# Performance work log

Measured on AMD Instinct MI355X. Metric: run time of the kernel, lower is better.

Reference implementation:

```python
import jax, jax.numpy as jnp
import numpy as np

B, T, EMB = 2, 2048, 1024
H, D = 16, 64          # n_heads, head_dim; H*D == EMB
FF = 4 * EMB


def _ln(x, w, b, eps=1e-5):
    mu = jnp.mean(x, axis=-1, keepdims=True)
    var = jnp.var(x, axis=-1, keepdims=True)
    return (x - mu) * jax.lax.rsqrt(var + eps) * w + b


def setup_inputs() -> dict:
    key = jax.random.key(0)
    ks = jax.random.split(key, 5)
    s = 0.02
    return {
        "x": jax.random.normal(ks[0], (B, T, EMB), jnp.float32),
        "ln1_w": jnp.ones((EMB,), jnp.float32),
        "ln1_b": jnp.zeros((EMB,), jnp.float32),
        "c_proj_w": jax.random.normal(ks[1], (3 * H * D, EMB), jnp.float32) * s,  # Linear(emb, 3HD, bias=False)
        "proj_w": jax.random.normal(ks[2], (EMB, H * D), jnp.float32) * s,
        "proj_b": jnp.zeros((EMB,), jnp.float32),
        "ln2_w": jnp.ones((EMB,), jnp.float32),
        "ln2_b": jnp.zeros((EMB,), jnp.float32),
        "ffn1_w": jax.random.normal(ks[3], (FF, EMB), jnp.float32) * s,
        "ffn1_b": jnp.zeros((FF,), jnp.float32),
        "ffn2_w": jax.random.normal(ks[4], (EMB, FF), jnp.float32) * s,
        "ffn2_b": jnp.zeros((EMB,), jnp.float32),
    }


def reference(x, ln1_w, ln1_b, c_proj_w, proj_w, proj_b, ln2_w, ln2_b,
              ffn1_w, ffn1_b, ffn2_w, ffn2_b):
    Bx, Tx, C = x.shape
    ln_x = _ln(x, ln1_w, ln1_b)
    c = ln_x @ c_proj_w.T                     # (B,T,3HD)
    c = c.reshape(Bx, Tx, H, 3 * D)
    k, q, v = jnp.split(c, 3, axis=-1)        # split order k,q,v as in source
    q = q.transpose(0, 2, 1, 3)               # (B,H,T,D)
    k = k.transpose(0, 2, 1, 3)
    v = v.transpose(0, 2, 1, 3)
    wei = jnp.einsum('bhqd,bhkd->bhqk', q, k) * (D ** -0.5)  # (B,H,T,T)
    mask = jnp.tril(jnp.ones((Tx, Tx), bool))
    wei = jnp.where(mask, wei, -jnp.inf)
    wei = jax.nn.softmax(wei, axis=-1)
    act = jnp.einsum('bhqk,bhkd->bhqd', wei, v)
    act = act.transpose(0, 2, 1, 3).reshape(Bx, Tx, H * D)
    act = act @ proj_w.T + proj_b
    act = x + act                              # residual 1
    h = _ln(act, ln2_w, ln2_b)
    h = jax.nn.relu(h @ ffn1_w.T + ffn1_b) @ ffn2_w.T + ffn2_b
    return x + h                               # NOTE: source adds x, not act
```

## Files before the change

### kernel.cpp

```cpp
#include <hip/hip_runtime.h>
#include <math.h>

typedef unsigned short u16;
typedef unsigned int u32;
typedef __attribute__((ext_vector_type(8))) __bf16 bf16x8;
typedef __attribute__((ext_vector_type(4))) float f32x4;
typedef __attribute__((ext_vector_type(16))) float f32x16;

#define DEVI __device__ __forceinline__

DEVI u16 f2bf(float f){
  u32 b = __builtin_bit_cast(u32, f);
  return (u16)((b + 0x7FFFu + ((b >> 16) & 1u)) >> 16);
}

DEVI u32 cvtpk(float a, float b){
  u32 r;
  asm("v_cvt_pk_bf16_f32 %0, %1, %2" : "=v"(r) : "v"(a), "v"(b));
  return r;
}

DEVI f32x4 mfma16(bf16x8 a, bf16x8 b, f32x4 c){
  return __builtin_amdgcn_mfma_f32_16x16x32_bf16(a, b, c, 0, 0, 0);
}
DEVI f32x16 mfma32(bf16x8 a, bf16x8 b, f32x16 c){
  return __builtin_amdgcn_mfma_f32_32x32x16_bf16(a, b, c, 0, 0, 0);
}

DEVI void gload16(const u16* g, u16* l){
  __builtin_amdgcn_global_load_lds(
      (const __attribute__((address_space(1))) u32*)g,
      (__attribute__((address_space(3))) u32*)l,
      16, 0, 0);
}

DEVI void phase_bar(){
  __builtin_amdgcn_sched_barrier(0);
  __builtin_amdgcn_s_barrier();
  __builtin_amdgcn_sched_barrier(0);
}

DEVI bf16x8 scale_bf16x8(bf16x8 v, float s){
  u32 w[4]; __builtin_memcpy(w, &v, 16);
  u32 o[4];
  #pragma unroll
  for (int i = 0; i < 4; ++i){
    float f0 = __builtin_bit_cast(float, (w[i] & 0xFFFFu) << 16) * s;
    float f1 = __builtin_bit_cast(float, w[i] & 0xFFFF0000u) * s;
    o[i] = (u32)f2bf(f0) | ((u32)f2bf(f1) << 16);
  }
  bf16x8 r; __builtin_memcpy(&r, o, 16);
  return r;
}

DEVI void cvt_body(const float* __restrict__ in, u16* __restrict__ out, int i){
  float4 v = reinterpret_cast<const float4*>(in)[i];
  u32 lo = (u32)f2bf(v.x) | ((u32)f2bf(v.y) << 16);
  u32 hi = (u32)f2bf(v.z) | ((u32)f2bf(v.w) << 16);
  reinterpret_cast<uint2*>(out)[i] = make_uint2(lo, hi);
}

DEVI void ln_body(const float* __restrict__ x, const float* __restrict__ w,
                  const float* __restrict__ b, u16* __restrict__ out,
                  int row, int tid, float* red){
  const float4 v = reinterpret_cast<const float4*>(x + (size_t)row * 1024)[tid];
  float s  = v.x + v.y + v.z + v.w;
  float ss = v.x*v.x + v.y*v.y + v.z*v.z + v.w*v.w;
  #pragma unroll
  for (int m = 1; m < 64; m <<= 1){
    s  += __shfl_xor(s,  m, 64);
    ss += __shfl_xor(ss, m, 64);
  }
  int wid = tid >> 6, lane = tid & 63;
  if (lane == 0){ red[wid] = s; red[4 + wid] = ss; }
  __syncthreads();
  s  = red[0] + red[1] + red[2] + red[3];
  ss = red[4] + red[5] + red[6] + red[7];
  float mu   = s * (1.0f/1024.0f);
  float var  = ss * (1.0f/1024.0f) - mu*mu;
  float rstd = rsqrtf(var + 1e-5f);
  const float4 wv = reinterpret_cast<const float4*>(w)[tid];
  const float4 bv = reinterpret_cast<const float4*>(b)[tid];
  u32 lo = (u32)f2bf((v.x-mu)*rstd*wv.x + bv.x) | ((u32)f2bf((v.y-mu)*rstd*wv.y + bv.y) << 16);
  u32 hi = (u32)f2bf((v.z-mu)*rstd*wv.z + bv.z) | ((u32)f2bf((v.w-mu)*rstd*wv.w + bv.w) << 16);
  reinterpret_cast<uint2*>(out + (size_t)row*1024)[tid] = make_uint2(lo, hi);
}

__global__ __launch_bounds__(256) void prep_kernel(const float* __restrict__ c_proj_w,
                                                   const float* __restrict__ proj_w,
                                                   const float* __restrict__ ffn1_w,
                                                   const float* __restrict__ ffn2_w,
                                                   const float* __restrict__ x,
                                                   const float* __restrict__ ln1_w,
                                                   const float* __restrict__ ln1_b,
                                                   u16* __restrict__ Wqkv,
                                                   u16* __restrict__ Wproj,
                                                   u16* __restrict__ Wff1,
                                                   u16* __restrict__ Wff2,
                                                   u16* __restrict__ LNb){
  __shared__ float red[8];
  const int bid = blockIdx.x;
  const int tid = threadIdx.x;
  if (bid < 3072){
    cvt_body(c_proj_w, Wqkv, bid*256 + tid);
  } else if (bid < 4096){
    cvt_body(proj_w, Wproj, (bid - 3072)*256 + tid);
  } else if (bid < 8192){
    cvt_body(ffn1_w, Wff1, (bid - 4096)*256 + tid);
  } else if (bid < 12288){
    cvt_body(ffn2_w, Wff2, (bid - 8192)*256 + tid);
  } else {
    ln_body(x, ln1_w, ln1_b, LNb, bid - 12288, tid, red);
  }
}

__global__ __launch_bounds__(256) void ln_kernel(const float* __restrict__ x,
                                                 const float* __restrict__ w,
                                                 const float* __restrict__ b,
                                                 u16* __restrict__ out){
  __shared__ float red[8];
  ln_body(x, w, b, out, blockIdx.x, threadIdx.x, red);
}

__global__ __launch_bounds__(256) void reduce4_kernel(const u16* __restrict__ P,
                                                      const float* __restrict__ x,
                                                      const float* __restrict__ bias,
                                                      float* __restrict__ out){
  const size_t i8 = ((size_t)blockIdx.x * 256 + threadIdx.x) * 8;
  const size_t PS = (size_t)4096 * 1024;
  const int col0 = (int)(i8 & 1023);
  float acc[8];
  #pragma unroll
  for (int j = 0; j < 8; ++j) acc[j] = bias[col0 + j];
  #pragma unroll
  for (int s = 0; s < 4; ++s){
    uint4 d = *reinterpret_cast<const uint4*>(P + s*PS + i8);
    u32 w[4] = {d.x, d.y, d.z, d.w};
    #pragma unroll
    for (int j = 0; j < 8; ++j){
      u32 bits = ((w[j>>1] >> (16*(j&1))) & 0xFFFFu) << 16;
      acc[j] += __builtin_bit_cast(float, bits);
    }
  }
  float4 xv0 = reinterpret_cast<const float4*>(x + i8)[0];
  float4 xv1 = reinterpret_cast<const float4*>(x + i8)[1];
  acc[0]+=xv0.x; acc[1]+=xv0.y; acc[2]+=xv0.z; acc[3]+=xv0.w;
  acc[4]+=xv1.x; acc[5]+=xv1.y; acc[6]+=xv1.z; acc[7]+=xv1.w;
  reinterpret_cast<float4*>(out + i8)[0] = make_float4(acc[0],acc[1],acc[2],acc[3]);
  reinterpret_cast<float4*>(out + i8)[1] = make_float4(acc[4],acc[5],acc[6],acc[7]);
}

template<bool HAS_BIAS, bool RELU, bool SPLIT>
__global__ __launch_bounds__(512, 2) void gemm256(const u16* __restrict__ A,
                                                  const u16* __restrict__ W,
                                                  const float* __restrict__ bias,
                                                  u16* __restrict__ outp,
                                                  int M, int N, int lda, int kLen){
  const int tid = threadIdx.x;
  const int wid = tid >> 6, lane = tid & 63;
  const int l16 = lane & 15, lhi = lane >> 4;
  const int wr = wid >> 2, wc = wid & 3;

  const int gx = gridDim.x, gy = gridDim.y;
  const int nwg = gx * gy * gridDim.z;
  const int bid = (blockIdx.z * gy + blockIdx.y) * gx + blockIdx.x;
  const int swz = (bid & 7) * (nwg >> 3) + (bid >> 3);
  const int col = swz % gx;
  const int rs  = swz / gx;
  const int row = rs % gy;
  const int ksp = rs / gy;
  const int brow = row * 256;
  const int bcol = col * 256;
  const size_t koff = (size_t)ksp * kLen;
  if (SPLIT) outp += (size_t)ksp * M * N;

  __shared__ u16 LDS[2][2][2][256*32];

  const int srow = tid >> 2;
  const int cg   = (tid & 3) ^ ((tid >> 3) & 3);
  const u16* gA = A + (size_t)(brow + srow) * lda + koff + cg*8;
  const u16* gW = W + (size_t)(bcol + srow) * lda + koff + cg*8;
  const size_t rK = (size_t)128 * lda;

#define STAGE(buf, mat, ks, t) do {                                   \
    const u16* _s = ((mat) ? gW : gA) + (t)*64 + (ks)*32;             \
    u16* _d = &LDS[buf][mat][ks][(wid*16)*32];                        \
    gload16(_s,      _d);                                             \
    gload16(_s + rK, _d + 128*32);                                    \
  } while(0)

  const int cswz = (lhi ^ ((l16 >> 1) & 3)) * 8;
  const int aoff = (wr*128 + l16)*32 + cswz;
  const int boff = (wc*64  + l16)*32 + cswz;
#define RDA(buf, ks, m) (*reinterpret_cast<const bf16x8*>(&LDS[buf][0][ks][aoff + (m)*512]))
#define RDB(buf, ks, n) (*reinterpret_cast<const bf16x8*>(&LDS[buf][1][ks][boff + (n)*512]))

  f32x4 acc[8][4] = {};
  bf16x8 a[8], b0, b1;

#define MFMA_PH(n0, n1) do {                                          \
    __builtin_amdgcn_s_setprio(1);                                    \
    _Pragma("unroll")                                                 \
    for (int m = 0; m < 8; ++m){                                      \
      acc[m][n0] = mfma16(a[m], b0, acc[m][n0]);                      \
      acc[m][n1] = mfma16(a[m], b1, acc[m][n1]);                      \
    }                                                                 \
    __builtin_amdgcn_s_setprio(0);                                    \
  } while(0)

  const int NITER = kLen >> 7;

  STAGE(0,0,0,0); STAGE(0,1,0,0); STAGE(0,0,1,0); STAGE(0,1,1,0);
  STAGE(1,0,0,1); STAGE(1,1,0,1);
  asm volatile("s_waitcnt vmcnt(4)" ::: "memory");
  phase_bar();

  for (int j = 0; j < NITER; ++j){
    const int t0 = 2*j, t1 = 2*j + 1;
    const bool more = (j + 1 < NITER);

    #pragma unroll
    for (int m = 0; m < 8; ++m) a[m] = RDA(0,0,m);
    b0 = RDB(0,0,0); b1 = RDB(0,0,1);
    STAGE(1,0,1,t1);
    phase_bar();
    MFMA_PH(0,1);
    phase_bar();
    b0 = RDB(0,0,2); b1 = RDB(0,0,3);
    STAGE(1,1,1,t1);
    phase_bar();
    MFMA_PH(2,3);
    phase_bar();
    #pragma unroll
    for (int m = 0; m < 8; ++m) a[m] = RDA(0,1,m);
    b0 = RDB(0,1,0); b1 = RDB(0,1,1);
    if (more) STAGE(0,0,0,t0+2);
    phase_bar();
    MFMA_PH(0,1);
    phase_bar();
    b0 = RDB(0,1,2); b1 = RDB(0,1,3);
    if (more){ STAGE(0,1,0,t0+2); asm volatile("s_waitcnt vmcnt(4)" ::: "memory"); }
    else     {                    asm volatile("s_waitcnt vmcnt(0)" ::: "memory"); }
    phase_bar();
    MFMA_PH(2,3);
    phase_bar();
    #pragma unroll
    for (int m = 0; m < 8; ++m) a[m] = RDA(1,0,m);
    b0 = RDB(1,0,0); b1 = RDB(1,0,1);
    if (more) STAGE(0,0,1,t0+2);
    phase_bar();
    MFMA_PH(0,1);
    phase_bar();
    b0 = RDB(1,0,2); b1 = RDB(1,0,3);
    if (more) STAGE(0,1,1,t0+2);
    phase_bar();
    MFMA_PH(2,3);
    phase_bar();
    #pragma unroll
    for (int m = 0; m < 8; ++m) a[m] = RDA(1,1,m);
    b0 = RDB(1,1,0); b1 = RDB(1,1,1);
    if (more) STAGE(1,0,0,t1+2);
    phase_bar();
    MFMA_PH(0,1);
    phase_bar();
    b0 = RDB(1,1,2); b1 = RDB(1,1,3);
    if (more){ STAGE(1,1,0,t1+2); asm volatile("s_waitcnt vmcnt(4)" ::: "memory"); }
    phase_bar();
    MFMA_PH(2,3);
    phase_bar();
  }
  __builtin_amdgcn_sched_barrier(0);

  const int row0 = brow + wr*128;
  const int col0 = bcol + wc*64;
  #pragma unroll
  for (int m = 0; m < 8; ++m){
    #pragma unroll
    for (int n = 0; n < 4; ++n){
      #pragma unroll
      for (int r = 0; r < 4; ++r){
        int row_ = row0 + m*16 + 4*lhi + r;
        int col_ = col0 + n*16 + l16;
        float v = acc[m][n][r];
        if constexpr (HAS_BIAS) v += bias[col_];
        if constexpr (RELU)     v = fmaxf(v, 0.0f);
        outp[(size_t)row_ * N + col_] = f2bf(v);
      }
    }
  }
#undef STAGE
#undef RDA
#undef RDB
#undef MFMA_PH
}

template<bool HAS_BIAS, bool HAS_RES, bool RELU, bool OUT_BF16>
__global__ __launch_bounds__(256) void gemm_bt(const u16* __restrict__ A,
                                               const u16* __restrict__ W,
                                               const float* __restrict__ bias,
                                               const float* __restrict__ res,
                                               void* __restrict__ outp,
                                               int M, int N, int K){
  const int tid = threadIdx.x;
  const int wid = tid >> 6, lane = tid & 63;
  const int l16 = lane & 15, lhi = lane >> 4;
  const int wr = wid >> 1, wc = wid & 1;

  const int gx = gridDim.x;
  const int nwg = gx * gridDim.y;
  const int bid = blockIdx.y * gx + blockIdx.x;
  const int swz = (bid & 7) * (nwg >> 3) + (bid >> 3);
  const int brow = (swz / gx) * 128;
  const int bcol = (swz % gx) * 128;

  __shared__ u16 As[2][128*32];
  __shared__ u16 Bs[2][128*32];

  const int srow = wid*32 + (lane >> 2);
  const int schk = lane & 3;
  const u16* gA0 = A + (size_t)(brow + srow)      * K + schk*8;
  const u16* gA1 = A + (size_t)(brow + srow + 16) * K + schk*8;
  const u16* gW0 = W + (size_t)(bcol + srow)      * K + schk*8;
  const u16* gW1 = W + (size_t)(bcol + srow + 16) * K + schk*8;
  const int ldsA0 = (wid*32)*32, ldsA1 = (wid*32 + 16)*32;

  f32x4 acc[4][4] = {};

  gload16(gA0, &As[0][ldsA0]);
  gload16(gA1, &As[0][ldsA1]);
  gload16(gW0, &Bs[0][ldsA0]);
  gload16(gW1, &Bs[0][ldsA1]);

  int cur = 0;
  for (int k0 = 0; k0 < K; k0 += 32){
    __syncthreads();
    if (k0 + 32 < K){
      gload16(gA0 + k0 + 32, &As[cur^1][ldsA0]);
      gload16(gA1 + k0 + 32, &As[cur^1][ldsA1]);
      gload16(gW0 + k0 + 32, &Bs[cur^1][ldsA0]);
      gload16(gW1 + k0 + 32, &Bs[cur^1][ldsA1]);
    }
    bf16x8 af[4], bfr[4];
    #pragma unroll
    for (int m = 0; m < 4; ++m)
      af[m]  = *reinterpret_cast<const bf16x8*>(&As[cur][(wr*64 + m*16 + l16)*32 + 8*lhi]);
    #pragma unroll
    for (int n = 0; n < 4; ++n)
      bfr[n] = *reinterpret_cast<const bf16x8*>(&Bs[cur][(wc*64 + n*16 + l16)*32 + 8*lhi]);
    #pragma unroll
    for (int m = 0; m < 4; ++m){
      #pragma unroll
      for (int n = 0; n < 4; ++n){
        acc[m][n] = mfma16(af[m], bfr[n], acc[m][n]);
      }
    }
    cur ^= 1;
  }

  const int row0 = brow + wr*64;
  const int col0 = bcol + wc*64;
  #pragma unroll
  for (int m = 0; m < 4; ++m){
    #pragma unroll
    for (int n = 0; n < 4; ++n){
      #pragma unroll
      for (int r = 0; r < 4; ++r){
        int row = row0 + m*16 + 4*lhi + r;
        int col = col0 + n*16 + l16;
        float v = acc[m][n][r];
        if constexpr (HAS_BIAS) v += bias[col];
        if constexpr (RELU)     v = fmaxf(v, 0.0f);
        if constexpr (HAS_RES)  v += res[(size_t)row * N + col];
        if constexpr (OUT_BF16) ((u16*)outp)[(size_t)row * N + col] = f2bf(v);
        else                    ((float*)outp)[(size_t)row * N + col] = v;
      }
    }
  }
}

__global__ __launch_bounds__(128) void attn_kernel(const u16* __restrict__ qkv,
                                                   u16* __restrict__ att){
  const int bh = blockIdx.x;
  const int g  = 31 - blockIdx.y;
  const int bb = bh >> 4, hh = bh & 15;
  const int tid = threadIdx.x;
  const int wid = tid >> 6, lane = tid & 63;
  const int l31 = lane & 31, h = lane >> 5;
  const u16* base = qkv + (size_t)bb * 2048 * 3072 + (size_t)hh * 192;

  __shared__ u16 Ks[2][64*72];
  __shared__ u16 Vt[2][64*80];

  const int sr = tid >> 1, sh2 = (tid & 1) * 32;
  const u16* kstage = base + (size_t)sr * 3072 + sh2;
  const int va = tid >> 2, vd = (tid & 3) * 16;
  const u16* vstage = base + (size_t)(2*va) * 3072 + 128 + vd;

  const int qrow0 = g*64 + wid*32;
  const int q = qrow0 + l31;

  const float QSCALE = 0.125f * 1.44269504f;
  bf16x8 qb[4];
  {
    const u16* qp = base + (size_t)q * 3072 + 64 + 8*h;
    #pragma unroll
    for (int s = 0; s < 4; ++s)
      qb[s] = scale_bf16x8(*reinterpret_cast<const bf16x8*>(qp + 16*s), QSCALE);
  }

  f32x16 o0 = (f32x16)0.0f, o1 = (f32x16)0.0f;
  float m = -INFINITY, l = 0.0f;

  const int nkt = g + 1;

  uint4 ka0, ka1, ka2, ka3, v00, v01, v10, v11;
#define LOADREGS(t) do {                                               \
    const u16* kp = kstage + (size_t)(t) * 64 * 3072;                  \
    const u16* vp = vstage + (size_t)(t) * 64 * 3072;                  \
    ka0 = *reinterpret_cast<const uint4*>(kp);                         \
    ka1 = *reinterpret_cast<const uint4*>(kp + 8);                     \
    ka2 = *reinterpret_cast<const uint4*>(kp + 16);                    \
    ka3 = *reinterpret_cast<const uint4*>(kp + 24);                    \
    v00 = *reinterpret_cast<const uint4*>(vp);                         \
    v01 = *reinterpret_cast<const uint4*>(vp + 8);                     \
    v10 = *reinterpret_cast<const uint4*>(vp + 3072);                  \
    v11 = *reinterpret_cast<const uint4*>(vp + 3072 + 8);              \
  } while(0)

#define WRITE_TILE(B) do {                                             \
    *reinterpret_cast<uint4*>(&Ks[B][sr*72 + sh2])      = ka0;         \
    *reinterpret_cast<uint4*>(&Ks[B][sr*72 + sh2 + 8])  = ka1;         \
    *reinterpret_cast<uint4*>(&Ks[B][sr*72 + sh2 + 16]) = ka2;         \
    *reinterpret_cast<uint4*>(&Ks[B][sr*72 + sh2 + 24]) = ka3;         \
    u32 w00[4] = {v00.x, v00.y, v00.z, v00.w};                         \
    u32 w01[4] = {v01.x, v01.y, v01.z, v01.w};                         \
    u32 w10[4] = {v10.x, v10.y, v10.z, v10.w};                         \
    u32 w11[4] = {v11.x, v11.y, v11.z, v11.w};                         \
    _Pragma("unroll")                                                  \
    for (int j = 0; j < 16; ++j){                                      \
      u32 e0 = ((j < 8 ? w00[j>>1] : w01[(j-8)>>1]) >> (16*(j&1))) & 0xFFFFu; \
      u32 e1 = ((j < 8 ? w10[j>>1] : w11[(j-8)>>1]) >> (16*(j&1))) & 0xFFFFu; \
      int d = vd + j;                                                  \
      *reinterpret_cast<u32*>(&Vt[B][d*80 + (((va>>2) ^ (d>>3)) << 3) + 2*(va&3)]) = \
          e0 | (e1 << 16);                                             \
    }                                                                  \
  } while(0)

  LOADREGS(0);
  WRITE_TILE(0);
  __syncthreads();
  if (nkt > 1) LOADREGS(1);

  for (int kt = 0; kt < nkt; ++kt){
    const int cur = kt & 1;

    if (kt + 1 < nkt){
      WRITE_TILE(cur ^ 1);
      if (kt + 2 < nkt) LOADREGS(kt + 2);
    }

    const u16* KsC = &Ks[cur][0];
    const u16* VtC = &Vt[cur][0];

    f32x16 s0 = (f32x16)0.0f, s1 = (f32x16)0.0f;
    __builtin_amdgcn_s_setprio(1);
    #pragma unroll
    for (int s = 0; s < 4; ++s){
      bf16x8 kf0 = *reinterpret_cast<const bf16x8*>(&KsC[l31*72      + 16*s + 8*h]);
      bf16x8 kf1 = *reinterpret_cast<const bf16x8*>(&KsC[(32+l31)*72 + 16*s + 8*h]);
      s0 = mfma32(kf0, qb[s], s0);
      s1 = mfma32(kf1, qb[s], s1);
    }
    __builtin_amdgcn_s_setprio(0);

    if (kt == nkt - 1){
      #pragma unroll
      for (int r = 0; r < 16; ++r){
        int krow = kt*64 + (r&3) + 8*(r>>2) + 4*h;
        if (krow > q)      s0[r] = -INFINITY;
        if (krow + 32 > q) s1[r] = -INFINITY;
      }
    }

    float mx = s0[0];
    #pragma unroll
    for (int r = 1; r < 16; ++r) mx = fmaxf(mx, s0[r]);
    #pragma unroll
    for (int r = 0; r < 16; ++r) mx = fmaxf(mx, s1[r]);
    mx = fmaxf(mx, __shfl_xor(mx, 32, 64));
    if (__any(mx > m)){
      float mnew = fmaxf(m, mx);
      float al = exp2f(m - mnew);
      m = mnew;
      l *= al;
      o0 *= al;
      o1 *= al;
    }
    float p0[16], p1[16];
    float su = 0.0f;
    #pragma unroll
    for (int r = 0; r < 16; ++r){ p0[r] = exp2f(s0[r] - m); su += p0[r]; }
    #pragma unroll
    for (int r = 0; r < 16; ++r){ p1[r] = exp2f(s1[r] - m); su += p1[r]; }
    l += su;

    u32 pk0[8], pk1[8];
    #pragma unroll
    for (int g4 = 0; g4 < 4; ++g4){
      pk0[2*g4]   = cvtpk(p0[4*g4],   p0[4*g4+1]);
      pk0[2*g4+1] = cvtpk(p0[4*g4+2], p0[4*g4+3]);
      pk1[2*g4]   = cvtpk(p1[4*g4],   p1[4*g4+1]);
      pk1[2*g4+1] = cvtpk(p1[4*g4+2], p1[4*g4+3]);
    }

    __builtin_amdgcn_s_setprio(1);
    #pragma unroll
    for (int s = 0; s < 4; ++s){
      const int gA = (s & 1) * 2;
      u32 oa0 = (s >> 1) ? pk1[2*gA]       : pk0[2*gA];
      u32 oa1 = (s >> 1) ? pk1[2*gA+1]     : pk0[2*gA+1];
      u32 ob0 = (s >> 1) ? pk1[2*(gA+1)]   : pk0[2*(gA+1)];
      u32 ob1 = (s >> 1) ? pk1[2*(gA+1)+1] : pk0[2*(gA+1)+1];
      u32 t0 = h ? oa0 : ob0;
      u32 t1 = h ? oa1 : ob1;
      u32 r0 = (u32)__shfl_xor((int)t0, 32, 64);
      u32 r1 = (u32)__shfl_xor((int)t1, 32, 64);
      u32 b0_ = h ? r0 : oa0;
      u32 b1_ = h ? r1 : oa1;
      u32 b2_ = h ? ob0 : r0;
      u32 b3_ = h ? ob1 : r1;
      bf16x8 pfrag = __builtin_bit_cast(bf16x8, make_uint4(b0_, b1_, b2_, b3_));
      bf16x8 vf0 = *reinterpret_cast<const bf16x8*>(
          &VtC[l31*80      + (((2*s + h) ^ (l31 >> 3)) << 3)]);
      bf16x8 vf1 = *reinterpret_cast<const bf16x8*>(
          &VtC[(32+l31)*80 + (((2*s + h) ^ ((32+l31) >> 3)) << 3)]);
      o0 = mfma32(vf0, pfrag, o0);
      o1 = mfma32(vf1, pfrag, o1);
    }
    __builtin_amdgcn_s_setprio(0);

    __syncthreads();
  }

  l += __shfl_xor(l, 32, 64);
  float inv = 1.0f / l;
  u16* orow = att + (size_t)(bb*2048 + q) * 1024 + hh*64;
  #pragma unroll
  for (int r = 0; r < 16; r += 2){
    int d0 = (r&3) + 8*(r>>2) + 4*h;
    *reinterpret_cast<u32*>(&orow[d0])      = cvtpk(o0[r]*inv, o0[r+1]*inv);
    *reinterpret_cast<u32*>(&orow[32 + d0]) = cvtpk(o1[r]*inv, o1[r+1]*inv);
  }
#undef LOADREGS
#undef WRITE_TILE
}

extern "C" void kernel_launch(void* const* d_in, const int* in_sizes, int n_in,
                              void* d_out, int out_size, void* d_ws, size_t ws_size,
                              hipStream_t stream){
  const float* x        = (const float*)d_in[0];
  const float* ln1_w    = (const float*)d_in[1];
  const float* ln1_b    = (const float*)d_in[2];
  const float* c_proj_w = (const float*)d_in[3];
  const float* proj_w   = (const float*)d_in[4];
  const float* proj_b   = (const float*)d_in[5];
  const float* ln2_w    = (const float*)d_in[6];
  const float* ln2_b    = (const float*)d_in[7];
  const float* ffn1_w   = (const float*)d_in[8];
  const float* ffn1_b   = (const float*)d_in[9];
  const float* ffn2_w   = (const float*)d_in[10];
  const float* ffn2_b   = (const float*)d_in[11];

  char* p = (char*)d_ws;
  u16* Wff1  = (u16*)p;  p += (size_t)4096*1024*2;
  u16* Wff2  = (u16*)p;  p += (size_t)1024*4096*2;
  u16* QKV   = (u16*)p;  p += (size_t)4096*3072*2;
  u16* ATT   = (u16*)p;  p += (size_t)4096*1024*2;
  u16* Wqkv  = (u16*)p;  p += (size_t)3072*1024*2;
  u16* Wproj = (u16*)p;  p += (size_t)1024*1024*2;
  u16* LNb   = (u16*)p;  p += (size_t)4096*1024*2;
  float* ACT2= (float*)p;
  u16* FFN1  = QKV;
  u16* PART  = Wqkv;

  prep_kernel<<<16384, 256, 0, stream>>>(c_proj_w, proj_w, ffn1_w, ffn2_w,
                                         x, ln1_w, ln1_b,
                                         Wqkv, Wproj, Wff1, Wff2, LNb);
  gemm256<false,false,false><<<dim3(12,16,1), 512, 0, stream>>>(LNb, Wqkv, nullptr, QKV, 4096, 3072, 1024, 1024);
  attn_kernel<<<dim3(32,32), 128, 0, stream>>>(QKV, ATT);
  gemm_bt<true ,true ,false,false><<<dim3(8,32), 256, 0, stream>>>(ATT, Wproj, proj_b, x, ACT2, 4096, 1024, 1024);
  ln_kernel<<<4096, 256, 0, stream>>>(ACT2, ln2_w, ln2_b, LNb);
  gemm256<true ,true ,false><<<dim3(16,16,1), 512, 0, stream>>>(LNb, Wff1, ffn1_b, FFN1, 4096, 4096, 1024, 1024);
  gemm256<false,false,true ><<<dim3(4,16,4), 512, 0, stream>>>(FFN1, Wff2, nullptr, PART, 4096, 1024, 4096, 1024);
  reduce4_kernel<<<2048, 256, 0, stream>>>(PART, x, ffn2_b, (float*)d_out);
}
```

Measured before the change: 235.7 us.

## Split attention KV range across two wave pairs and merge partial softmax states

The attention block grows from 128 to 256 threads. Each pair of waves now processes half of the causal KV tiles for the same 64 query rows, and the two partial (m, l, O) states are combined through shared memory at the end, split-K style. The goal is shorter per-block serial KV loops and more waves in flight to reduce causal tail imbalance. In exchange, the double-buffered register-to-LDS prefetch is replaced by a single buffer per half with two barriers per iteration, which weakens overlap of loads with compute. It also adds a shared-memory reduction step.

```diff
diff --git a/kernel.cpp b/kernel.cpp
--- a/kernel.cpp
+++ b/kernel.cpp
@@ -378,25 +378,28 @@
   }
 }
 
-__global__ __launch_bounds__(128) void attn_kernel(const u16* __restrict__ qkv,
+__global__ __launch_bounds__(256) void attn_kernel(const u16* __restrict__ qkv,
                                                    u16* __restrict__ att){
   const int bh = blockIdx.x;
   const int g  = 31 - blockIdx.y;
   const int bb = bh >> 4, hh = bh & 15;
   const int tid = threadIdx.x;
   const int wid = tid >> 6, lane = tid & 63;
+  const int half = wid >> 1;
+  const int p    = wid & 1;
   const int l31 = lane & 31, h = lane >> 5;
   const u16* base = qkv + (size_t)bb * 2048 * 3072 + (size_t)hh * 192;
 
-  __shared__ u16 Ks[2][64*72];
-  __shared__ u16 Vt[2][64*80];
-
-  const int sr = tid >> 1, sh2 = (tid & 1) * 32;
+  __shared__ __align__(16) u16 Ks[2][64*72];
+  __shared__ __align__(16) u16 Vt[2][64*80];
+
+  const int th = tid & 127;
+  const int sr = th >> 1, sh2 = (th & 1) * 32;
   const u16* kstage = base + (size_t)sr * 3072 + sh2;
-  const int va = tid >> 2, vd = (tid & 3) * 16;
+  const int va = th >> 2, vd = (th & 3) * 16;
   const u16* vstage = base + (size_t)(2*va) * 3072 + 128 + vd;
 
-  const int qrow0 = g*64 + wid*32;
+  const int qrow0 = g*64 + p*32;
   const int q = qrow0 + l31;
 
   const float QSCALE = 0.125f * 1.44269504f;
@@ -411,7 +414,9 @@
   f32x16 o0 = (f32x16)0.0f, o1 = (f32x16)0.0f;
   float m = -INFINITY, l = 0.0f;
 
-  const int nkt = g + 1;
+  const int h0  = (g + 2) >> 1;
+  const int lo  = half ? h0 : 0;
+  const int len = half ? (g + 1 - h0) : h0;
 
   uint4 ka0, ka1, ka2, ka3, v00, v01, v10, v11;
 #define LOADREGS(t) do {                                               \
@@ -427,40 +432,39 @@
     v11 = *reinterpret_cast<const uint4*>(vp + 3072 + 8);              \
   } while(0)
 
-#define WRITE_TILE(B) do {                                             \
-    *reinterpret_cast<uint4*>(&Ks[B][sr*72 + sh2])      = ka0;         \
-    *reinterpret_cast<uint4*>(&Ks[B][sr*72 + sh2 + 8])  = ka1;         \
-    *reinterpret_cast<uint4*>(&Ks[B][sr*72 + sh2 + 16]) = ka2;         \
-    *reinterpret_cast<uint4*>(&Ks[B][sr*72 + sh2 + 24]) = ka3;         \
-    u32 w00[4] = {v00.x, v00.y, v00.z, v00.w};                         \
-    u32 w01[4] = {v01.x, v01.y, v01.z, v01.w};                         \
-    u32 w10[4] = {v10.x, v10.y, v10.z, v10.w};                         \
-    u32 w11[4] = {v11.x, v11.y, v11.z, v11.w};                         \
-    _Pragma("unroll")                                                  \
-    for (int j = 0; j < 16; ++j){                                      \
-      u32 e0 = ((j < 8 ? w00[j>>1] : w01[(j-8)>>1]) >> (16*(j&1))) & 0xFFFFu; \
-      u32 e1 = ((j < 8 ? w10[j>>1] : w11[(j-8)>>1]) >> (16*(j&1))) & 0xFFFFu; \
-      int d = vd + j;                                                  \
-      *reinterpret_cast<u32*>(&Vt[B][d*80 + (((va>>2) ^ (d>>3)) << 3) + 2*(va&3)]) = \
-          e0 | (e1 << 16);                                             \
-    }                                                                  \
-  } while(0)
-
-  LOADREGS(0);
-  WRITE_TILE(0);
-  __syncthreads();
-  if (nkt > 1) LOADREGS(1);
-
-  for (int kt = 0; kt < nkt; ++kt){
-    const int cur = kt & 1;
-
-    if (kt + 1 < nkt){
-      WRITE_TILE(cur ^ 1);
-      if (kt + 2 < nkt) LOADREGS(kt + 2);
-    }
-
-    const u16* KsC = &Ks[cur][0];
-    const u16* VtC = &Vt[cur][0];
+  if (len > 0) LOADREGS(lo);
+
+  for (int it = 0; it < h0; ++it){
+    const int kt = lo + it;
+    const bool act = it < len;
+
+    __syncthreads();
+    if (act){
+      *reinterpret_cast<uint4*>(&Ks[half][sr*72 + sh2])      = ka0;
+      *reinterpret_cast<uint4*>(&Ks[half][sr*72 + sh2 + 8])  = ka1;
+      *reinterpret_cast<uint4*>(&Ks[half][sr*72 + sh2 + 16]) = ka2;
+      *reinterpret_cast<uint4*>(&Ks[half][sr*72 + sh2 + 24]) = ka3;
+      u32 w00[4] = {v00.x, v00.y, v00.z, v00.w};
+      u32 w01[4] = {v01.x, v01.y, v01.z, v01.w};
+      u32 w10[4] = {v10.x, v10.y, v10.z, v10.w};
+      u32 w11[4] = {v11.x, v11.y, v11.z, v11.w};
+      #pragma unroll
+      for (int j = 0; j < 16; ++j){
+        u32 e0 = ((j < 8 ? w00[j>>1] : w01[(j-8)>>1]) >> (16*(j&1))) & 0xFFFFu;
+        u32 e1 = ((j < 8 ? w10[j>>1] : w11[(j-8)>>1]) >> (16*(j&1))) & 0xFFFFu;
+        int d = vd + j;
+        *reinterpret_cast<u32*>(&Vt[half][d*80 + (((va>>2) ^ (d>>3)) << 3) + 2*(va&3)]) =
+            e0 | (e1 << 16);
+      }
+    }
+    __syncthreads();
+
+    if (!act) continue;
+
+    if (it + 1 < len) LOADREGS(kt + 1);
+
+    const u16* KsC = &Ks[half][0];
+    const u16* VtC = &Vt[half][0];
 
     f32x16 s0 = (f32x16)0.0f, s1 = (f32x16)0.0f;
     __builtin_amdgcn_s_setprio(1);
@@ -473,7 +477,7 @@
     }
     __builtin_amdgcn_s_setprio(0);
 
-    if (kt == nkt - 1){
+    if (kt == g){
       #pragma unroll
       for (int r = 0; r < 16; ++r){
         int krow = kt*64 + (r&3) + 8*(r>>2) + 4*h;
@@ -538,21 +542,44 @@
       o1 = mfma32(vf1, pfrag, o1);
     }
     __builtin_amdgcn_s_setprio(0);
-
-    __syncthreads();
-  }
+  }
+
+  __syncthreads();
+  float* ob  = (float*)&Ks[0][0];
+  float* mlb = (float*)&Vt[0][0];
+  const int pl = p*64 + lane;
 
   l += __shfl_xor(l, 32, 64);
-  float inv = 1.0f / l;
-  u16* orow = att + (size_t)(bb*2048 + q) * 1024 + hh*64;
-  #pragma unroll
-  for (int r = 0; r < 16; r += 2){
-    int d0 = (r&3) + 8*(r>>2) + 4*h;
-    *reinterpret_cast<u32*>(&orow[d0])      = cvtpk(o0[r]*inv, o0[r+1]*inv);
-    *reinterpret_cast<u32*>(&orow[32 + d0]) = cvtpk(o1[r]*inv, o1[r+1]*inv);
+
+  if (half == 1){
+    #pragma unroll
+    for (int r = 0; r < 16; ++r){
+      ob[r*128 + pl]        = o0[r];
+      ob[(16 + r)*128 + pl] = o1[r];
+    }
+    mlb[pl*2]     = m;
+    mlb[pl*2 + 1] = l;
+  }
+  __syncthreads();
+  if (half == 0){
+    float mB = mlb[pl*2], lB = mlb[pl*2 + 1];
+    float mS = fmaxf(m, mB);
+    float sA = exp2f(m - mS), sB = exp2f(mB - mS);
+    float inv = 1.0f / (l*sA + lB*sB);
+    sA *= inv; sB *= inv;
+    u16* orow = att + (size_t)(bb*2048 + q) * 1024 + hh*64;
+    #pragma unroll
+    for (int r = 0; r < 16; r += 2){
+      int d0 = (r&3) + 8*(r>>2) + 4*h;
+      float a0 = o0[r]*sA     + ob[r*128 + pl]*sB;
+      float a1 = o0[r+1]*sA   + ob[(r+1)*128 + pl]*sB;
+      float c0 = o1[r]*sA     + ob[(16+r)*128 + pl]*sB;
+      float c1 = o1[r+1]*sA   + ob[(16+r+1)*128 + pl]*sB;
+      *reinterpret_cast<u32*>(&orow[d0])      = cvtpk(a0, a1);
+      *reinterpret_cast<u32*>(&orow[32 + d0]) = cvtpk(c0, c1);
+    }
   }
 #undef LOADREGS
-#undef WRITE_TILE
 }
 
 extern "C" void kernel_launch(void* const* d_in, const int* in_sizes, int n_in,
@@ -587,7 +614,7 @@
                                          x, ln1_w, ln1_b,
                                          Wqkv, Wproj, Wff1, Wff2, LNb);
   gemm256<false,false,false><<<dim3(12,16,1), 512, 0, stream>>>(LNb, Wqkv, nullptr, QKV, 4096, 3072, 1024, 1024);
-  attn_kernel<<<dim3(32,32), 128, 0, stream>>>(QKV, ATT);
+  attn_kernel<<<dim3(32,32), 256, 0, stream>>>(QKV, ATT);
   gemm_bt<true ,true ,false,false><<<dim3(8,32), 256, 0, stream>>>(ATT, Wproj, proj_b, x, ACT2, 4096, 1024, 1024);
   ln_kernel<<<4096, 256, 0, stream>>>(ACT2, ln2_w, ln2_b, LNb);
   gemm256<true ,true ,false><<<dim3(16,16,1), 512, 0, stream>>>(LNb, Wff1, ffn1_b, FFN1, 4096, 4096, 1024, 1024);
```

New measurement: 225.8 us. 4.2% less time.
